# Performance work log

Measured on AMD Instinct MI355X. Metric: run time of the kernel, lower is better.

Reference implementation:

```python
import jax, jax.numpy as jnp
import numpy as np

D_MODEL = 768
N_HEADS = 12
HEAD_DIM = D_MODEL // N_HEADS


def rotary_emb(seq_len, dim):
    # matches RotaryEmbedding: emb = concat(sin(freqs), cos(freqs)) over last dim
    inv_freq = 1.0 / (10000.0 ** (jnp.arange(0, dim, 2, dtype=jnp.float32) / dim))
    t = jnp.arange(seq_len, dtype=jnp.float32)
    freqs = t[:, None] * inv_freq[None, :]            # [T, dim/2]
    return jnp.concatenate([jnp.sin(freqs), jnp.cos(freqs)], axis=-1)  # [T, dim]


def apply_rotary_pos_emb(x, emb):
    # faithful to the source's (quirky) interleaved slicing of the concat'd emb
    x1, x2 = x[..., ::2], x[..., 1::2]
    sin, cos = emb[..., ::2], emb[..., 1::2]
    return jnp.concatenate([x1 * cos - x2 * sin, x1 * sin + x2 * cos], axis=-1)


def setup_inputs() -> dict:
    key = jax.random.key(0)
    ks = jax.random.split(key, 14)
    B, Tq, Tk = 2, 2048, 4096
    s = 1.0 / np.sqrt(D_MODEL)
    return {
        "query": jax.random.normal(ks[0], (B, Tq, D_MODEL), jnp.float32),
        "key": jax.random.normal(ks[1], (B, Tk, D_MODEL), jnp.float32),
        "value": jax.random.normal(ks[2], (B, Tk, D_MODEL), jnp.float32),
        "Wq": jax.random.normal(ks[3], (D_MODEL, D_MODEL), jnp.float32) * s,
        "bq": jnp.zeros((D_MODEL,), jnp.float32),
        "Wk": jax.random.normal(ks[4], (D_MODEL, D_MODEL), jnp.float32) * s,
        "bk": jnp.zeros((D_MODEL,), jnp.float32),
        "Wv": jax.random.normal(ks[5], (D_MODEL, D_MODEL), jnp.float32) * s,
        "bv": jnp.zeros((D_MODEL,), jnp.float32),
        "Wo": jax.random.normal(ks[6], (D_MODEL, D_MODEL), jnp.float32) * s,
        "bo": jnp.zeros((D_MODEL,), jnp.float32),
    }


def reference(query, key, value, Wq, bq, Wk, bk, Wv, bv, Wo, bo):
    B, Tq, _ = query.shape
    Tk = key.shape[1]
    H, D = N_HEADS, HEAD_DIM

    q = (query @ Wq.T + bq).reshape(B, Tq, H, D).transpose(0, 2, 1, 3)  # [B,H,Tq,D]
    k = (key @ Wk.T + bk).reshape(B, Tk, H, D).transpose(0, 2, 1, 3)    # [B,H,Tk,D]
    v = (value @ Wv.T + bv).reshape(B, Tk, H, D).transpose(0, 2, 1, 3)  # [B,H,Tk,D]

    q = apply_rotary_pos_emb(q, rotary_emb(Tq, D)[None, None, :, :])
    k = apply_rotary_pos_emb(k, rotary_emb(Tk, D)[None, None, :, :])

    scores = jnp.einsum("bhqd,bhkd->bhqk", q, k) / jnp.sqrt(jnp.float32(D))
    weights = jax.nn.softmax(scores, axis=-1)
    attn = jnp.einsum("bhqk,bhkd->bhqd", weights, v)  # [B,H,Tq,D]

    out = attn.transpose(0, 2, 1, 3).reshape(B, Tq, H * D)
    return out @ Wo.T + bo
```

## Files before the change

### kernel.cpp

```cpp
#include <hip/hip_runtime.h>
#include <hip/hip_bf16.h>
#include <math.h>

#define DM 768
#define HEADS 12
#define BQ 2
#define TQ 2048
#define TK 4096
#define NSPLIT 4
#define KTS (TK / 64 / NSPLIT)
#define ROWS (BQ * HEADS * TQ)

typedef __attribute__((ext_vector_type(8))) short bf16x8;
typedef __attribute__((ext_vector_type(4))) float f32x4;
typedef __attribute__((ext_vector_type(16))) float f32x16;
typedef __attribute__((ext_vector_type(4))) short short4v;
typedef __attribute__((ext_vector_type(2))) unsigned uint2v;

__device__ inline unsigned pk2bf(float a, float b) {
    union { __hip_bfloat162 h; unsigned u; } c;
    c.h = __float22bfloat162_rn(make_float2(a, b));
    return c.u;
}
__device__ inline short f2bf(float f) { return (short)(pk2bf(f, f) & 0xffffu); }

__device__ inline float bf2f(short s) {
    union { unsigned u; float f; } a; a.u = ((unsigned)(unsigned short)s) << 16;
    return a.f;
}

__device__ inline void plswap(unsigned &a, unsigned &b) {
    uint2v r = __builtin_amdgcn_permlane32_swap(a, b, false, false);
    a = r[0]; b = r[1];
}
__device__ inline void plswap2(unsigned &a, unsigned &b, unsigned x) {
    uint2v r = __builtin_amdgcn_permlane32_swap(x, x, false, false);
    a = r[0]; b = r[1];
}

__global__ void rope_tables(float2* scu) {
    int idx = blockIdx.x * 256 + threadIdx.x;
    if (idx >= TK * 32) return;
    int t = idx >> 5, j = idx & 31;
    double su, cu;
    if (j < 16) {
        su = sin((double)t * pow(10000.0, -(double)(2 * (2 * j)) / 64.0));
        cu = sin((double)t * pow(10000.0, -(double)(2 * (2 * j + 1)) / 64.0));
    } else {
        su = cos((double)t * pow(10000.0, -(double)(2 * (2 * j - 32)) / 64.0));
        cu = cos((double)t * pow(10000.0, -(double)(2 * (2 * j - 31)) / 64.0));
    }
    scu[idx] = make_float2((float)su, (float)cu);
}

__global__ __launch_bounds__(256) void gemm_qkv(
        const float* __restrict__ query, const float* __restrict__ key_,
        const float* __restrict__ value,
        const float* __restrict__ Wq, const float* __restrict__ bq,
        const float* __restrict__ Wk, const float* __restrict__ bk,
        const float* __restrict__ Wv, const float* __restrict__ bv,
        const float2* __restrict__ scu,
        short* __restrict__ qh, short* __restrict__ kh, short* __restrict__ vt,
        float qscale) {
    __shared__ short Alds[128 * 40];
    __shared__ short Blds[128 * 40];
    const int tid = threadIdx.x;
    const int lane = tid & 63, wid = tid >> 6;
    const int wr = wid >> 1, wc = wid & 1;
    const int l4 = lane >> 4, l15 = lane & 15;
    const int bx = blockIdx.x, bn = blockIdx.y * 128;

    const float* X; const float* W; const float* bias;
    short* dst; int bm, tsh, mode; float scale;
    if (bx < 32)      { X = query; W = Wq; bias = bq; dst = qh; bm = bx * 128;        tsh = 11; mode = 0; scale = qscale; }
    else if (bx < 96) { X = key_;  W = Wk; bias = bk; dst = kh; bm = (bx - 32) * 128; tsh = 12; mode = 0; scale = 1.f; }
    else              { X = value; W = Wv; bias = bv; dst = vt; bm = (bx - 96) * 128; tsh = 12; mode = 1; scale = 1.f; }
    const int T = 1 << tsh, tmask = T - 1;

    int srow[4], skq[4];
#pragma unroll
    for (int p = 0; p < 4; ++p) {
        int c = p * 256 + tid;
        srow[p] = c >> 3; skq[p] = (c & 7) * 4;
    }

    f32x4 acc[4][4] = {};
    float4 fa[4], fw[4];

#pragma unroll
    for (int p = 0; p < 4; ++p) {
        fa[p] = *reinterpret_cast<const float4*>(&X[(size_t)(bm + srow[p]) * DM + skq[p]]);
        fw[p] = *reinterpret_cast<const float4*>(&W[(size_t)(bn + srow[p]) * DM + skq[p]]);
    }

    for (int k0 = 0; k0 < DM; k0 += 32) {
#pragma unroll
        for (int p = 0; p < 4; ++p) {
            uint2v s; s.x = pk2bf(fa[p].x, fa[p].y); s.y = pk2bf(fa[p].z, fa[p].w);
            *reinterpret_cast<uint2v*>(&Alds[srow[p] * 40 + skq[p]]) = s;
            uint2v t4; t4.x = pk2bf(fw[p].x, fw[p].y); t4.y = pk2bf(fw[p].z, fw[p].w);
            *reinterpret_cast<uint2v*>(&Blds[srow[p] * 40 + skq[p]]) = t4;
        }
        __syncthreads();

        if (k0 + 32 < DM) {
#pragma unroll
            for (int p = 0; p < 4; ++p) {
                fa[p] = *reinterpret_cast<const float4*>(&X[(size_t)(bm + srow[p]) * DM + k0 + 32 + skq[p]]);
                fw[p] = *reinterpret_cast<const float4*>(&W[(size_t)(bn + srow[p]) * DM + k0 + 32 + skq[p]]);
            }
        }

        bf16x8 af[4], bfr[4];
#pragma unroll
        for (int i = 0; i < 4; ++i)
            af[i] = *reinterpret_cast<const bf16x8*>(&Alds[(wr * 64 + i * 16 + l15) * 40 + l4 * 8]);
#pragma unroll
        for (int j = 0; j < 4; ++j)
            bfr[j] = *reinterpret_cast<const bf16x8*>(&Blds[(wc * 64 + j * 16 + l15) * 40 + l4 * 8]);
        __builtin_amdgcn_s_setprio(1);
#pragma unroll
        for (int i = 0; i < 4; ++i)
#pragma unroll
            for (int j = 0; j < 4; ++j)
                acc[i][j] = __builtin_amdgcn_mfma_f32_16x16x32_bf16(af[i], bfr[j], acc[i][j], 0, 0, 0);
        __builtin_amdgcn_s_setprio(0);
        __syncthreads();
    }

    if (mode == 0) {
#pragma unroll
        for (int i = 0; i < 4; ++i) {
            int mrow0 = bm + wr * 64 + i * 16 + l4 * 4;
#pragma unroll
            for (int j = 0; j < 4; ++j) {
                int n = bn + wc * 64 + j * 16 + l15;
                int hh = n >> 6, c = n & 63, u = c >> 1, odd = c & 1;
                float bb = bias[n];
#pragma unroll
                for (int r = 0; r < 4; ++r) {
                    float val = acc[i][j][r] + bb;
                    float pv = __shfl_xor(val, 1);
                    int mrow = mrow0 + r;
                    int b_ = mrow >> tsh, t = mrow & tmask;
                    float2 sc = scu[t * 32 + u];
                    float outv = odd ? (pv * sc.x + val * sc.y)
                                     : (val * sc.y - pv * sc.x);
                    int d = (odd << 5) + u;
                    dst[((size_t)(b_ * HEADS + hh) * T + t) * 64 + d] = f2bf(outv * scale);
                }
            }
        }
    } else {
#pragma unroll
        for (int i = 0; i < 4; ++i) {
            int mrow0 = bm + wr * 64 + i * 16 + l4 * 4;
            int b_ = mrow0 >> 12, t = mrow0 & 4095;
#pragma unroll
            for (int j = 0; j < 4; ++j) {
                int n = bn + wc * 64 + j * 16 + l15;
                int hh = n >> 6, dd = n & 63;
                float bb = bias[n];
                uint2v s;
                s.x = pk2bf(acc[i][j][0] + bb, acc[i][j][1] + bb);
                s.y = pk2bf(acc[i][j][2] + bb, acc[i][j][3] + bb);
                *reinterpret_cast<uint2v*>(
                    &dst[((size_t)(b_ * HEADS + hh) * 64 + dd) * TK + t]) = s;
            }
        }
    }
}

__global__ __launch_bounds__(256) void gemm_out(const short* __restrict__ Xh,
                                                const float* __restrict__ W,
                                                const float* __restrict__ bias,
                                                float* __restrict__ Y) {
    __shared__ short Alds[128 * 40];
    __shared__ short Blds[128 * 40];
    const int tid = threadIdx.x;
    const int lane = tid & 63, wid = tid >> 6;
    const int wr = wid >> 1, wc = wid & 1;
    const int l4 = lane >> 4, l15 = lane & 15;
    const int bm = blockIdx.x * 128, bn = blockIdx.y * 128;

    int srow[4], skq[4];
#pragma unroll
    for (int p = 0; p < 4; ++p) {
        int c = p * 256 + tid;
        srow[p] = c >> 3; skq[p] = (c & 7) * 4;
    }

    f32x4 acc[4][4] = {};
    short4v ra[4]; float4 fw[4];

#pragma unroll
    for (int p = 0; p < 4; ++p) {
        ra[p] = *reinterpret_cast<const short4v*>(&Xh[(size_t)(bm + srow[p]) * DM + skq[p]]);
        fw[p] = *reinterpret_cast<const float4*>(&W[(size_t)(bn + srow[p]) * DM + skq[p]]);
    }

    for (int k0 = 0; k0 < DM; k0 += 32) {
#pragma unroll
        for (int p = 0; p < 4; ++p) {
            *reinterpret_cast<short4v*>(&Alds[srow[p] * 40 + skq[p]]) = ra[p];
            uint2v t4; t4.x = pk2bf(fw[p].x, fw[p].y); t4.y = pk2bf(fw[p].z, fw[p].w);
            *reinterpret_cast<uint2v*>(&Blds[srow[p] * 40 + skq[p]]) = t4;
        }
        __syncthreads();

        if (k0 + 32 < DM) {
#pragma unroll
            for (int p = 0; p < 4; ++p) {
                ra[p] = *reinterpret_cast<const short4v*>(&Xh[(size_t)(bm + srow[p]) * DM + k0 + 32 + skq[p]]);
                fw[p] = *reinterpret_cast<const float4*>(&W[(size_t)(bn + srow[p]) * DM + k0 + 32 + skq[p]]);
            }
        }

        bf16x8 af[4], bfr[4];
#pragma unroll
        for (int i = 0; i < 4; ++i)
            af[i] = *reinterpret_cast<const bf16x8*>(&Alds[(wr * 64 + i * 16 + l15) * 40 + l4 * 8]);
#pragma unroll
        for (int j = 0; j < 4; ++j)
            bfr[j] = *reinterpret_cast<const bf16x8*>(&Blds[(wc * 64 + j * 16 + l15) * 40 + l4 * 8]);
        __builtin_amdgcn_s_setprio(1);
#pragma unroll
        for (int i = 0; i < 4; ++i)
#pragma unroll
            for (int j = 0; j < 4; ++j)
                acc[i][j] = __builtin_amdgcn_mfma_f32_16x16x32_bf16(af[i], bfr[j], acc[i][j], 0, 0, 0);
        __builtin_amdgcn_s_setprio(0);
        __syncthreads();
    }

#pragma unroll
    for (int i = 0; i < 4; ++i) {
        int m = bm + wr * 64 + i * 16 + l4 * 4;
#pragma unroll
        for (int j = 0; j < 4; ++j) {
            int n = bn + wc * 64 + j * 16 + l15;
            float bb = bias[n];
#pragma unroll
            for (int r = 0; r < 4; ++r)
                Y[(size_t)(m + r) * DM + n] = acc[i][j][r] + bb;
        }
    }
}

__global__ __launch_bounds__(512) void attn(const short* __restrict__ qh,
                                            const short* __restrict__ kh,
                                            const short* __restrict__ vt,
                                            short* __restrict__ Opart,
                                            float* __restrict__ ml) {
    __shared__ short Ks[2][64 * 64];
    __shared__ short Vs[2][64 * 64];
    const int id = blockIdx.x;
    const int hs = id % 96, qt = id / 96;
    const int h = hs % HEADS, rest = hs / HEADS;
    const int split = rest & 3, b = rest >> 2;
    const int tid = threadIdx.x, lane = tid & 63, w = tid >> 6;
    const int l31 = lane & 31, hi = lane >> 5;
    const size_t bh = (size_t)(b * HEADS + h);
    const short* kbase = kh + bh * TK * 64;
    const short* vbase = vt + bh * (size_t)64 * TK;
    const int t0 = split * KTS;

#define SWZ(row, bo) ((row) * 64 + ((((bo)) ^ (((row) & 7) << 4)) >> 1))
#define KGLB(c, t_) (kbase + ((size_t)(t_) * 64 + ((c) >> 3)) * 64 + ((c) & 7) * 8)
#define VGLB(c, t_) (vbase + (size_t)((c) >> 3) * TK + (t_) * 64 + ((c) & 7) * 8)

    int loff[2][4];
#pragma unroll
    for (int t2 = 0; t2 < 2; ++t2)
#pragma unroll
        for (int d0 = 0; d0 < 4; ++d0)
            loff[t2][d0] = SWZ(t2 * 32 + l31, d0 * 32 + hi * 16);

    bf16x8 qf[4];
    {
        const short* qrow = qh + (bh * TQ + (size_t)qt * 256 + w * 32 + l31) * 64 + hi * 8;
#pragma unroll
        for (int d0 = 0; d0 < 4; ++d0)
            qf[d0] = *reinterpret_cast<const bf16x8*>(qrow + d0 * 16);
    }

    f32x16 oacc[2] = {};
    float lsum = 0.f;

    const int c0 = tid;
    const int sw0 = SWZ(c0 >> 3, (c0 & 7) * 16);

    {
        bf16x8 k0 = *reinterpret_cast<const bf16x8*>(KGLB(c0, t0));
        bf16x8 v0 = *reinterpret_cast<const bf16x8*>(VGLB(c0, t0));
        *reinterpret_cast<bf16x8*>(&Ks[0][sw0]) = k0;
        *reinterpret_cast<bf16x8*>(&Vs[0][sw0]) = v0;
    }
    __syncthreads();

    int cur = 0;
    for (int kt = 0; kt < KTS; ++kt) {
        const bool pre = (kt + 1 < KTS);
        bf16x8 sk0, sv0;
        if (pre) {
            sk0 = *reinterpret_cast<const bf16x8*>(KGLB(c0, t0 + kt + 1));
            sv0 = *reinterpret_cast<const bf16x8*>(VGLB(c0, t0 + kt + 1));
        }

        f32x16 sacc[2] = {};
        __builtin_amdgcn_s_setprio(1);
#pragma unroll
        for (int t2 = 0; t2 < 2; ++t2)
#pragma unroll
            for (int d0 = 0; d0 < 4; ++d0) {
                bf16x8 kf = *reinterpret_cast<const bf16x8*>(&Ks[cur][loff[t2][d0]]);
                sacc[t2] = __builtin_amdgcn_mfma_f32_32x32x16_bf16(kf, qf[d0], sacc[t2], 0, 0, 0);
            }
        __builtin_amdgcn_s_setprio(0);

#pragma unroll
        for (int t2 = 0; t2 < 2; ++t2)
#pragma unroll
            for (int i = 0; i < 16; ++i)
                sacc[t2][i] = exp2f(sacc[t2][i]);
        float s8[8];
#pragma unroll
        for (int i = 0; i < 8; ++i)
            s8[i] = (sacc[0][i] + sacc[0][i + 8]) + (sacc[1][i] + sacc[1][i + 8]);
        float rs = ((s8[0] + s8[1]) + (s8[2] + s8[3])) + ((s8[4] + s8[5]) + (s8[6] + s8[7]));
        {
            unsigned a, bb2;
            plswap2(a, bb2, __float_as_uint(rs));
            rs = __uint_as_float(a) + __uint_as_float(bb2);
        }
        lsum += rs;

#define PP(idx) (sacc[(idx) >> 4][(idx) & 15])
        bf16x8 pa[4];
#pragma unroll
        for (int ks = 0; ks < 4; ++ks) {
            const int base = (ks >> 1) * 16 + (ks & 1) * 8;
            unsigned u0 = pk2bf(PP(base + 0), PP(base + 1));
            unsigned u1 = pk2bf(PP(base + 2), PP(base + 3));
            unsigned u2 = pk2bf(PP(base + 4), PP(base + 5));
            unsigned u3 = pk2bf(PP(base + 6), PP(base + 7));
            plswap(u0, u2);
            plswap(u1, u3);
            union { unsigned u[4]; bf16x8 v; } asm_;
            asm_.u[0] = u0; asm_.u[1] = u1; asm_.u[2] = u2; asm_.u[3] = u3;
            pa[ks] = asm_.v;
        }
#undef PP

        if (pre) {
            *reinterpret_cast<bf16x8*>(&Ks[cur ^ 1][sw0]) = sk0;
            *reinterpret_cast<bf16x8*>(&Vs[cur ^ 1][sw0]) = sv0;
        }

        __builtin_amdgcn_s_setprio(1);
#pragma unroll
        for (int dt = 0; dt < 2; ++dt)
#pragma unroll
            for (int ks = 0; ks < 4; ++ks) {
                bf16x8 vf = *reinterpret_cast<const bf16x8*>(&Vs[cur][loff[dt][ks]]);
                oacc[dt] = __builtin_amdgcn_mfma_f32_32x32x16_bf16(vf, pa[ks], oacc[dt], 0, 0, 0);
            }
        __builtin_amdgcn_s_setprio(0);

        __syncthreads();
        cur ^= 1;
    }

    float rln = 1.f / lsum;
    const size_t R = bh * TQ + (size_t)qt * 256 + w * 32 + l31;
    const size_t obase = ((size_t)split * ROWS + R) * 64;
#pragma unroll
    for (int dt = 0; dt < 2; ++dt)
#pragma unroll
        for (int rq = 0; rq < 4; ++rq) {
            uint2v st;
            st.x = pk2bf(oacc[dt][rq * 4 + 0] * rln, oacc[dt][rq * 4 + 1] * rln);
            st.y = pk2bf(oacc[dt][rq * 4 + 2] * rln, oacc[dt][rq * 4 + 3] * rln);
            *reinterpret_cast<uint2v*>(&Opart[obase + dt * 32 + rq * 8 + hi * 4]) = st;
        }
    if (hi == 0)
        ml[(size_t)split * ROWS + R] = lsum;
#undef SWZ
#undef KGLB
#undef VGLB
}

__global__ __launch_bounds__(256) void attn_combine(const short* __restrict__ Opart,
                                                    const float* __restrict__ ml,
                                                    short* __restrict__ attnO) {
    int idx = blockIdx.x * 256 + threadIdx.x;
    int R = idx >> 3, g = idx & 7;
    float wgt[NSPLIT], L = 0.f;
#pragma unroll
    for (int s = 0; s < NSPLIT; ++s) {
        wgt[s] = ml[(size_t)s * ROWS + R];
        L += wgt[s];
    }
    float rL = 1.f / L;
    float o[8] = {};
#pragma unroll
    for (int s = 0; s < NSPLIT; ++s) {
        float c = wgt[s] * rL;
        bf16x8 v = *reinterpret_cast<const bf16x8*>(&Opart[(((size_t)s * ROWS + R) * 64) + g * 8]);
#pragma unroll
        for (int i = 0; i < 8; ++i) o[i] += c * bf2f(v[i]);
    }
    int bh = R >> 11, t = R & 2047;
    int b = bh / HEADS, h = bh - b * HEADS;
    uint2v s0, s1;
    s0.x = pk2bf(o[0], o[1]); s0.y = pk2bf(o[2], o[3]);
    s1.x = pk2bf(o[4], o[5]); s1.y = pk2bf(o[6], o[7]);
    size_t dst = (((size_t)b * TQ + t) * HEADS + h) * 64 + g * 8;
    *reinterpret_cast<uint2v*>(&attnO[dst]) = s0;
    *reinterpret_cast<uint2v*>(&attnO[dst + 4]) = s1;
}

extern "C" void kernel_launch(void* const* d_in, const int* in_sizes, int n_in,
                              void* d_out, int out_size, void* d_ws, size_t ws_size,
                              hipStream_t stream) {
    const float* query = (const float*)d_in[0];
    const float* key_  = (const float*)d_in[1];
    const float* value = (const float*)d_in[2];
    const float* Wq = (const float*)d_in[3];
    const float* bq = (const float*)d_in[4];
    const float* Wk = (const float*)d_in[5];
    const float* bk = (const float*)d_in[6];
    const float* Wv = (const float*)d_in[7];
    const float* bv = (const float*)d_in[8];
    const float* Wo = (const float*)d_in[9];
    const float* bo = (const float*)d_in[10];
    float* out = (float*)d_out;

    char* ws = (char*)d_ws;
    float2* scu  = (float2*)(ws + 0);
    short* qh    = (short*)(ws + 1048576);
    short* kh    = (short*)(ws + 7340032);
    short* vt    = (short*)(ws + 19922944);
    short* attnO = (short*)(ws + 32505856);
    short* Opart = (short*)(ws + 38797312);
    float* ml    = (float*)(ws + 63963136);

    dim3 blk(256);
    const float QSCALE = 0.125f * 1.44269504088896341f;

    rope_tables<<<(TK * 32 + 255) / 256, blk, 0, stream>>>(scu);
    gemm_qkv<<<dim3(160, 6), blk, 0, stream>>>(query, key_, value, Wq, bq, Wk, bk,
                                               Wv, bv, scu, qh, kh, vt, QSCALE);
    attn<<<dim3(8 * 96), dim3(512), 0, stream>>>(qh, kh, vt, Opart, ml);
    attn_combine<<<ROWS * 8 / 256, blk, 0, stream>>>(Opart, ml, attnO);
    gemm_out<<<dim3(BQ * TQ / 128, DM / 128), blk, 0, stream>>>(attnO, Wo, bo, out);
}
```

Before: 187.5 us.

## Remap GEMM blocks per XCD and halve attention block size for occupancy

The GEMM kernels switch to a 1D grid whose block index is remapped so that consecutive blocks on each XCD share the same row tiles, which is meant to improve L2 reuse on the multi-die GPU. The attention kernel moves from 512 threads covering 256 query rows to 256 threads covering 128 query rows, with twice as many blocks and each thread loading two K/V chunks per tile. Launch bounds now request minimum occupancy (3 blocks for gemm_qkv, 4 for attn), which may cap registers and cause spills. Because attention blocks are smaller, each block loads K/V for fewer queries, so total K/V traffic per query rises.

```diff
diff --git a/kernel.cpp b/kernel.cpp
--- a/kernel.cpp
+++ b/kernel.cpp
@@ -53,7 +53,7 @@
     scu[idx] = make_float2((float)su, (float)cu);
 }
 
-__global__ __launch_bounds__(256) void gemm_qkv(
+__global__ __launch_bounds__(256, 3) void gemm_qkv(
         const float* __restrict__ query, const float* __restrict__ key_,
         const float* __restrict__ value,
         const float* __restrict__ Wq, const float* __restrict__ bq,
@@ -68,7 +68,10 @@
     const int lane = tid & 63, wid = tid >> 6;
     const int wr = wid >> 1, wc = wid & 1;
     const int l4 = lane >> 4, l15 = lane & 15;
-    const int bx = blockIdx.x, bn = blockIdx.y * 128;
+    const int id = blockIdx.x;
+    const int xcd = id & 7, pos = id >> 3;
+    const int bx = xcd * 20 + pos / 6;
+    const int bn = (pos % 6) * 128;
 
     const float* X; const float* W; const float* bias;
     short* dst; int bm, tsh, mode; float scale;
@@ -83,14 +86,16 @@
         int c = p * 256 + tid;
         srow[p] = c >> 3; skq[p] = (c & 7) * 4;
     }
+    const float* Xb = X + (size_t)bm * DM;
+    const float* Wb = W + (size_t)bn * DM;
 
     f32x4 acc[4][4] = {};
     float4 fa[4], fw[4];
 
 #pragma unroll
     for (int p = 0; p < 4; ++p) {
-        fa[p] = *reinterpret_cast<const float4*>(&X[(size_t)(bm + srow[p]) * DM + skq[p]]);
-        fw[p] = *reinterpret_cast<const float4*>(&W[(size_t)(bn + srow[p]) * DM + skq[p]]);
+        fa[p] = *reinterpret_cast<const float4*>(&Xb[(size_t)srow[p] * DM + skq[p]]);
+        fw[p] = *reinterpret_cast<const float4*>(&Wb[(size_t)srow[p] * DM + skq[p]]);
     }
 
     for (int k0 = 0; k0 < DM; k0 += 32) {
@@ -106,8 +111,8 @@
         if (k0 + 32 < DM) {
 #pragma unroll
             for (int p = 0; p < 4; ++p) {
-                fa[p] = *reinterpret_cast<const float4*>(&X[(size_t)(bm + srow[p]) * DM + k0 + 32 + skq[p]]);
-                fw[p] = *reinterpret_cast<const float4*>(&W[(size_t)(bn + srow[p]) * DM + k0 + 32 + skq[p]]);
+                fa[p] = *reinterpret_cast<const float4*>(&Xb[(size_t)srow[p] * DM + k0 + 32 + skq[p]]);
+                fw[p] = *reinterpret_cast<const float4*>(&Wb[(size_t)srow[p] * DM + k0 + 32 + skq[p]]);
             }
         }
 
@@ -181,7 +186,10 @@
     const int lane = tid & 63, wid = tid >> 6;
     const int wr = wid >> 1, wc = wid & 1;
     const int l4 = lane >> 4, l15 = lane & 15;
-    const int bm = blockIdx.x * 128, bn = blockIdx.y * 128;
+    const int id = blockIdx.x;
+    const int xcd = id & 7, pos = id >> 3;
+    const int bm = (xcd * 4 + pos / 6) * 128;
+    const int bn = (pos % 6) * 128;
 
     int srow[4], skq[4];
 #pragma unroll
@@ -247,11 +255,11 @@
     }
 }
 
-__global__ __launch_bounds__(512) void attn(const short* __restrict__ qh,
-                                            const short* __restrict__ kh,
-                                            const short* __restrict__ vt,
-                                            short* __restrict__ Opart,
-                                            float* __restrict__ ml) {
+__global__ __launch_bounds__(256, 4) void attn(const short* __restrict__ qh,
+                                               const short* __restrict__ kh,
+                                               const short* __restrict__ vt,
+                                               short* __restrict__ Opart,
+                                               float* __restrict__ ml) {
     __shared__ short Ks[2][64 * 64];
     __shared__ short Vs[2][64 * 64];
     const int id = blockIdx.x;
@@ -278,7 +286,7 @@
 
     bf16x8 qf[4];
     {
-        const short* qrow = qh + (bh * TQ + (size_t)qt * 256 + w * 32 + l31) * 64 + hi * 8;
+        const short* qrow = qh + (bh * TQ + (size_t)qt * 128 + w * 32 + l31) * 64 + hi * 8;
 #pragma unroll
         for (int d0 = 0; d0 < 4; ++d0)
             qf[d0] = *reinterpret_cast<const bf16x8*>(qrow + d0 * 16);
@@ -287,24 +295,30 @@
     f32x16 oacc[2] = {};
     float lsum = 0.f;
 
-    const int c0 = tid;
-    const int sw0 = SWZ(c0 >> 3, (c0 & 7) * 16);
+    const int c0 = tid, c1 = tid + 256;
+    const int sw0 = SWZ(c0 >> 3, (c0 & 7) * 16), sw1 = SWZ(c1 >> 3, (c1 & 7) * 16);
 
     {
         bf16x8 k0 = *reinterpret_cast<const bf16x8*>(KGLB(c0, t0));
+        bf16x8 k1 = *reinterpret_cast<const bf16x8*>(KGLB(c1, t0));
         bf16x8 v0 = *reinterpret_cast<const bf16x8*>(VGLB(c0, t0));
+        bf16x8 v1 = *reinterpret_cast<const bf16x8*>(VGLB(c1, t0));
         *reinterpret_cast<bf16x8*>(&Ks[0][sw0]) = k0;
+        *reinterpret_cast<bf16x8*>(&Ks[0][sw1]) = k1;
         *reinterpret_cast<bf16x8*>(&Vs[0][sw0]) = v0;
+        *reinterpret_cast<bf16x8*>(&Vs[0][sw1]) = v1;
     }
     __syncthreads();
 
     int cur = 0;
     for (int kt = 0; kt < KTS; ++kt) {
         const bool pre = (kt + 1 < KTS);
-        bf16x8 sk0, sv0;
+        bf16x8 sk0, sk1, sv0, sv1;
         if (pre) {
             sk0 = *reinterpret_cast<const bf16x8*>(KGLB(c0, t0 + kt + 1));
+            sk1 = *reinterpret_cast<const bf16x8*>(KGLB(c1, t0 + kt + 1));
             sv0 = *reinterpret_cast<const bf16x8*>(VGLB(c0, t0 + kt + 1));
+            sv1 = *reinterpret_cast<const bf16x8*>(VGLB(c1, t0 + kt + 1));
         }
 
         f32x16 sacc[2] = {};
@@ -354,7 +368,9 @@
 
         if (pre) {
             *reinterpret_cast<bf16x8*>(&Ks[cur ^ 1][sw0]) = sk0;
+            *reinterpret_cast<bf16x8*>(&Ks[cur ^ 1][sw1]) = sk1;
             *reinterpret_cast<bf16x8*>(&Vs[cur ^ 1][sw0]) = sv0;
+            *reinterpret_cast<bf16x8*>(&Vs[cur ^ 1][sw1]) = sv1;
         }
 
         __builtin_amdgcn_s_setprio(1);
@@ -372,7 +388,7 @@
     }
 
     float rln = 1.f / lsum;
-    const size_t R = bh * TQ + (size_t)qt * 256 + w * 32 + l31;
+    const size_t R = bh * TQ + (size_t)qt * 128 + w * 32 + l31;
     const size_t obase = ((size_t)split * ROWS + R) * 64;
 #pragma unroll
     for (int dt = 0; dt < 2; ++dt)
@@ -449,9 +465,9 @@
     const float QSCALE = 0.125f * 1.44269504088896341f;
 
     rope_tables<<<(TK * 32 + 255) / 256, blk, 0, stream>>>(scu);
-    gemm_qkv<<<dim3(160, 6), blk, 0, stream>>>(query, key_, value, Wq, bq, Wk, bk,
-                                               Wv, bv, scu, qh, kh, vt, QSCALE);
-    attn<<<dim3(8 * 96), dim3(512), 0, stream>>>(qh, kh, vt, Opart, ml);
+    gemm_qkv<<<dim3(960), blk, 0, stream>>>(query, key_, value, Wq, bq, Wk, bk,
+                                            Wv, bv, scu, qh, kh, vt, QSCALE);
+    attn<<<dim3(16 * 96), blk, 0, stream>>>(qh, kh, vt, Opart, ml);
     attn_combine<<<ROWS * 8 / 256, blk, 0, stream>>>(Opart, ml, attnO);
-    gemm_out<<<dim3(BQ * TQ / 128, DM / 128), blk, 0, stream>>>(attnO, Wo, bo, out);
-}
+    gemm_out<<<dim3(192), blk, 0, stream>>>(attnO, Wo, bo, out);
+}
```

Result: no change. 187.2 us (-0.2%).
